# Performance work log

Measured on AMD Instinct MI355X. Metric: run time of the kernel, lower is better.

Reference implementation:

```python
import jax, jax.numpy as jnp
import numpy as np
from functools import partial

E = 256   # input_size (embedding dim)
H = 256   # hidden_size
T = 4096  # number of admissions (GRU sequence length, batch=1)


def _gru_seq(x_seq, w_ih, w_hh, b_ih, b_hh):
    """Single-layer unidirectional GRU over x_seq [T, E] with batch=1.
    PyTorch gate order: r, z, n. Returns outputs [T, H]."""
    h_dim = w_hh.shape[1]
    # input projections are step-independent: precompute [T, 3H]
    gi_all = x_seq @ w_ih.T + b_ih

    def step(h, gi):
        gh = h @ w_hh.T + b_hh
        i_r, i_z, i_n = jnp.split(gi, 3)
        h_r, h_z, h_n = jnp.split(gh, 3)
        r = jax.nn.sigmoid(i_r + h_r)
        z = jax.nn.sigmoid(i_z + h_z)
        n = jnp.tanh(i_n + r * h_n)
        h_new = (1.0 - z) * n + z * h
        return h_new, h_new

    h0 = jnp.zeros((h_dim,), x_seq.dtype)
    _, out = jax.lax.scan(step, h0, gi_all)
    return out  # [T, H]


def setup_inputs() -> dict:
    key = jax.random.key(0)
    ks = jax.random.split(key, 16)
    u = lambda k, shape, s: jax.random.uniform(k, shape, jnp.float32, -s, s)
    sg = 1.0 / np.sqrt(H)  # PyTorch GRU/Linear init scale
    inp = {}
    # embeddings initialized uniform(-0.1, 0.1) per initialize_weights()
    inp["emb_diag"] = u(ks[0], (20000, E), 0.1)
    inp["emb_proc"] = u(ks[1], (15000, E), 0.1)  # unused by forward (source bug), kept for fidelity
    # GRU params (layer 0), gate order r,z,n
    inp["wih_d"] = u(ks[2], (3 * H, E), sg)
    inp["whh_d"] = u(ks[3], (3 * H, H), sg)
    inp["bih_d"] = u(ks[4], (3 * H,), sg)
    inp["bhh_d"] = u(ks[5], (3 * H,), sg)
    inp["wih_p"] = u(ks[6], (3 * H, E), sg)
    inp["whh_p"] = u(ks[7], (3 * H, H), sg)
    inp["bih_p"] = u(ks[8], (3 * H,), sg)
    inp["bhh_p"] = u(ks[9], (3 * H,), sg)
    # linear_embedding: ReLU -> Linear(2H, H)
    sl = 1.0 / np.sqrt(2 * H)
    inp["w_lin"] = u(ks[10], (H, 2 * H), sl)
    inp["b_lin"] = u(ks[11], (H,), sl)
    # ragged admission code lists, represented as fixed-length rows
    inp["diag_codes"] = jax.random.randint(ks[12], (T, 32), 0, 20000)
    inp["proc_codes"] = jax.random.randint(ks[13], (T, 16), 0, 15000)
    inp["input_medication"] = jax.random.randint(ks[14], (T, 24), 0, 3000)
    return inp


def reference(emb_diag, emb_proc, wih_d, whh_d, bih_d, bhh_d,
              wih_p, whh_p, bih_p, bhh_p, w_lin, b_lin,
              diag_codes, proc_codes, input_medication):
    # per-admission embedding gather + mean pool (dropout rate 0 -> identity)
    # NOTE: original source uses embedding_diagnoses for BOTH loops (bug kept).
    seq_d = emb_diag[diag_codes].mean(axis=1)  # [T, E]
    seq_p = emb_diag[proc_codes].mean(axis=1)  # [T, E]
    out_d = _gru_seq(seq_d, wih_d, whh_d, bih_d, bhh_d)  # [T, H]
    out_p = _gru_seq(seq_p, wih_p, whh_p, bih_p, bhh_p)  # [T, H]
    patient = jnp.concatenate([out_d, out_p], axis=-1)   # [T, 2H]
    queries = jax.nn.relu(patient) @ w_lin.T + b_lin     # [T, H]
    query = queries[-1:]
    memory_keys = queries[:-1]
    memory_values = input_medication[:-1]
    return (query, memory_keys, memory_values)
```

## Files before the change

### kernel.cpp

```cpp
#include <hip/hip_runtime.h>
#include <hip/hip_fp16.h>

#define T_SEQ 4096
#define E_DIM 256
#define H_DIM 256
#define G3    768

#define KEYS_OFF 256
#define MED_OFF  1048576

#define WS_SEQ_D   0
#define WS_SEQ_P   1048576
#define WS_GI_D    2097152
#define WS_GI_P    5242880
#define WS_PATIENT 8388608

#define SW_SCALE   2016.0f
#define SH_SCALE   127.0f
#define INV_SY     (1.0f / (2016.0f * 127.0f))

__device__ __forceinline__ float fast_rcp(float x) {
#if __has_builtin(__builtin_amdgcn_rcpf)
    return __builtin_amdgcn_rcpf(x);
#else
    return 1.f / x;
#endif
}

__device__ __forceinline__ int sdot4(int a, int b, int c) {
#if __has_builtin(__builtin_amdgcn_sdot4)
    return __builtin_amdgcn_sdot4(a, b, c, false);
#else
    c += ((a << 24) >> 24) * ((b << 24) >> 24);
    c += ((a << 16) >> 24) * ((b << 16) >> 24);
    c += ((a <<  8) >> 24) * ((b <<  8) >> 24);
    c += ( a        >> 24) * ( b        >> 24);
    return c;
#endif
}

__device__ __forceinline__ int quad_sum_i32(int x) {
#if __has_builtin(__builtin_amdgcn_update_dpp)
    x += __builtin_amdgcn_update_dpp(0, x, 0xB1 , 0xF, 0xF, true);
    x += __builtin_amdgcn_update_dpp(0, x, 0x4E , 0xF, 0xF, true);
    return x;
#else
    x += __shfl_xor(x, 1);
    x += __shfl_xor(x, 2);
    return x;
#endif
}

__global__ __launch_bounds__(256) void gather_mean_kernel(
    const float* __restrict__ emb, const int* __restrict__ dcodes,
    const int* __restrict__ pcodes, const int* __restrict__ med,
    float* __restrict__ seq_d, float* __restrict__ seq_p,
    float* __restrict__ med_out)
{
    const int t = blockIdx.x;
    const int e = threadIdx.x;
    __shared__ int cd[32];
    __shared__ int cp[16];
    if (e < 32) cd[e] = dcodes[t * 32 + e];
    else if (e < 48) cp[e - 32] = pcodes[t * 16 + (e - 32)];
    __syncthreads();

    float sd = 0.f;
#pragma unroll 4
    for (int i = 0; i < 32; i++) sd += emb[(size_t)cd[i] * E_DIM + e];
    seq_d[(size_t)t * E_DIM + e] = sd * (1.f / 32.f);

    float sp = 0.f;
#pragma unroll 4
    for (int i = 0; i < 16; i++) sp += emb[(size_t)cp[i] * E_DIM + e];
    seq_p[(size_t)t * E_DIM + e] = sp * (1.f / 16.f);

    if (t < T_SEQ - 1 && e < 24) med_out[t * 24 + e] = (float)med[t * 24 + e];
}

__global__ __launch_bounds__(256) void gemm_gi_kernel(
    const float* __restrict__ seq_d, const float* __restrict__ seq_p,
    const float* __restrict__ wih_d, const float* __restrict__ wih_p,
    const float* __restrict__ bih_d, const float* __restrict__ bih_p,
    float* __restrict__ gi_d, float* __restrict__ gi_p)
{
    const int K = E_DIM, N = G3;
    const float* A    = blockIdx.z ? seq_p : seq_d;
    const float* W    = blockIdx.z ? wih_p : wih_d;
    const float* bias = blockIdx.z ? bih_p : bih_d;
    float*       C    = blockIdx.z ? gi_p  : gi_d;

    __shared__ float As[16][132];
    __shared__ float Bs[16][132];

    const int tid = threadIdx.x;
    const int tx = tid & 15, ty = tid >> 4;
    const int m0 = blockIdx.x * 128, n0 = blockIdx.y * 128;
    const int r = tid >> 2;
    const int c = (tid & 3) << 2;

    float acc[8][8];
#pragma unroll
    for (int i = 0; i < 8; i++)
#pragma unroll
        for (int j = 0; j < 8; j++) acc[i][j] = 0.f;

    for (int k0 = 0; k0 < K; k0 += 16) {
        float4 a0 = *(const float4*)&A[(size_t)(m0 + r) * K + k0 + c];
        float4 a1 = *(const float4*)&A[(size_t)(m0 + r + 64) * K + k0 + c];
        float4 b0 = *(const float4*)&W[(size_t)(n0 + r) * K + k0 + c];
        float4 b1 = *(const float4*)&W[(size_t)(n0 + r + 64) * K + k0 + c];
        As[c + 0][r] = a0.x; As[c + 1][r] = a0.y; As[c + 2][r] = a0.z; As[c + 3][r] = a0.w;
        As[c + 0][r + 64] = a1.x; As[c + 1][r + 64] = a1.y; As[c + 2][r + 64] = a1.z; As[c + 3][r + 64] = a1.w;
        Bs[c + 0][r] = b0.x; Bs[c + 1][r] = b0.y; Bs[c + 2][r] = b0.z; Bs[c + 3][r] = b0.w;
        Bs[c + 0][r + 64] = b1.x; Bs[c + 1][r + 64] = b1.y; Bs[c + 2][r + 64] = b1.z; Bs[c + 3][r + 64] = b1.w;
        __syncthreads();
#pragma unroll
        for (int k = 0; k < 16; k++) {
            float4 aa0 = *(const float4*)&As[k][ty * 8];
            float4 aa1 = *(const float4*)&As[k][ty * 8 + 4];
            float4 bb0 = *(const float4*)&Bs[k][tx * 8];
            float4 bb1 = *(const float4*)&Bs[k][tx * 8 + 4];
            float a[8] = {aa0.x, aa0.y, aa0.z, aa0.w, aa1.x, aa1.y, aa1.z, aa1.w};
            float b[8] = {bb0.x, bb0.y, bb0.z, bb0.w, bb1.x, bb1.y, bb1.z, bb1.w};
#pragma unroll
            for (int i = 0; i < 8; i++)
#pragma unroll
                for (int j = 0; j < 8; j++) acc[i][j] = fmaf(a[i], b[j], acc[i][j]);
        }
        __syncthreads();
    }

#pragma unroll
    for (int i = 0; i < 8; i++) {
        const int m = m0 + ty * 8 + i;
#pragma unroll
        for (int j = 0; j < 8; j++) {
            const int n = n0 + tx * 8 + j;
            C[(size_t)m * N + n] = acc[i][j] + bias[n];
        }
    }
}

__global__ __launch_bounds__(256) void quant_whh_kernel(
    const float* __restrict__ whh_d, const float* __restrict__ whh_p,
    unsigned int* __restrict__ w8_d, unsigned int* __restrict__ w8_p)
{
    const int idx = blockIdx.x * 256 + threadIdx.x;
    const float* src = blockIdx.y ? whh_p : whh_d;
    unsigned int* dst = blockIdx.y ? w8_p : w8_d;
    const float4 f = *(const float4*)&src[(size_t)idx * 4];
    const int b0 = (int)rintf(f.x * SW_SCALE) & 0xFF;
    const int b1 = (int)rintf(f.y * SW_SCALE) & 0xFF;
    const int b2 = (int)rintf(f.z * SW_SCALE) & 0xFF;
    const int b3 = (int)rintf(f.w * SW_SCALE) & 0xFF;
    dst[idx] = (unsigned int)(b0 | (b1 << 8) | (b2 << 16) | (b3 << 24));
}

__global__ __launch_bounds__(1024, 4) void gru_scan_kernel(
    const unsigned int* __restrict__ w8_d, const unsigned int* __restrict__ w8_p,
    const float* __restrict__ bhh_d, const float* __restrict__ bhh_p,
    const float* __restrict__ gi_d, const float* __restrict__ gi_p,
    float* __restrict__ patient)
{
    const unsigned int* w8 = blockIdx.x ? w8_p : w8_d;
    const float* bhh = blockIdx.x ? bhh_p : bhh_d;
    const float* gi  = blockIdx.x ? gi_p  : gi_d;
    const int col_off = blockIdx.x ? H_DIM : 0;

    const int tid = threadIdx.x;
    const int q = tid >> 2;
    const int l = tid & 3;

    int wreg[3][16];
#pragma unroll
    for (int g = 0; g < 3; g++) {
        const int4* p = (const int4*)(w8 + ((size_t)(g * 256 + q) * 64 + l * 16));
#pragma unroll
        for (int i = 0; i < 4; i++) {
            const int4 v = p[i];
            wreg[g][4 * i + 0] = v.x;
            wreg[g][4 * i + 1] = v.y;
            wreg[g][4 * i + 2] = v.z;
            wreg[g][4 * i + 3] = v.w;
        }
    }

    __shared__ __align__(16) char hb[4 * 80];
    __shared__ int ylds[3 * 256];

    if (tid < 320) hb[tid] = 0;

    float h = 0.f, g0 = 0.f, g1 = 0.f, g2 = 0.f, b0 = 0.f, b1 = 0.f, b2 = 0.f;
    if (tid < H_DIM) {
        b0 = bhh[tid]; b1 = bhh[256 + tid]; b2 = bhh[512 + tid];
        g0 = gi[tid]; g1 = gi[256 + tid]; g2 = gi[512 + tid];
    }
    __syncthreads();

    const uint4* hp = (const uint4*)(hb + l * 80);

    for (int t = 0; t < T_SEQ; t++) {
        const uint4 H0 = hp[0], H1 = hp[1], H2 = hp[2], H3 = hp[3];
        int a0 = 0, a1 = 0, a2 = 0;
        {
            const int hd0 = (int)H0.x, hd1 = (int)H0.y, hd2 = (int)H0.z, hd3 = (int)H0.w;
            const int hd4 = (int)H1.x, hd5 = (int)H1.y, hd6 = (int)H1.z, hd7 = (int)H1.w;
            const int hd8 = (int)H2.x, hd9 = (int)H2.y, hd10 = (int)H2.z, hd11 = (int)H2.w;
            const int hd12 = (int)H3.x, hd13 = (int)H3.y, hd14 = (int)H3.z, hd15 = (int)H3.w;
#define DOT_G(A, G) \
            A = sdot4(wreg[G][0],  hd0,  A); A = sdot4(wreg[G][1],  hd1,  A); \
            A = sdot4(wreg[G][2],  hd2,  A); A = sdot4(wreg[G][3],  hd3,  A); \
            A = sdot4(wreg[G][4],  hd4,  A); A = sdot4(wreg[G][5],  hd5,  A); \
            A = sdot4(wreg[G][6],  hd6,  A); A = sdot4(wreg[G][7],  hd7,  A); \
            A = sdot4(wreg[G][8],  hd8,  A); A = sdot4(wreg[G][9],  hd9,  A); \
            A = sdot4(wreg[G][10], hd10, A); A = sdot4(wreg[G][11], hd11, A); \
            A = sdot4(wreg[G][12], hd12, A); A = sdot4(wreg[G][13], hd13, A); \
            A = sdot4(wreg[G][14], hd14, A); A = sdot4(wreg[G][15], hd15, A);
            DOT_G(a0, 0)
            DOT_G(a1, 1)
            DOT_G(a2, 2)
#undef DOT_G
        }
        a0 = quad_sum_i32(a0);
        a1 = quad_sum_i32(a1);
        a2 = quad_sum_i32(a2);
        if (l == 0) {
            ylds[q] = a0;
            ylds[256 + q] = a1;
            ylds[512 + q] = a2;
        }
        __syncthreads();

        if (tid < H_DIM) {
            const float y0 = (float)ylds[tid] * INV_SY;
            const float y1 = (float)ylds[256 + tid] * INV_SY;
            const float y2 = (float)ylds[512 + tid] * INV_SY;
            const float xr = g0 + y0 + b0;
            const float xz = g1 + y1 + b1;
            const float r = fast_rcp(1.f + __expf(-xr));
            const float z = fast_rcp(1.f + __expf(-xz));
            float xn = g2 + r * (y2 + b2);
            xn = fminf(fmaxf(xn, -15.f), 15.f);
            const float e2 = __expf(2.f * xn);
            const float n = (e2 - 1.f) * fast_rcp(e2 + 1.f);
            h = (1.f - z) * n + z * h;
            hb[(tid >> 6) * 80 + (tid & 63)] = (char)(int)rintf(h * SH_SCALE);
            patient[(size_t)t * 512 + col_off + tid] = h;
            const int tn = (t < T_SEQ - 1) ? (t + 1) : t;
            g0 = gi[(size_t)tn * G3 + tid];
            g1 = gi[(size_t)tn * G3 + 256 + tid];
            g2 = gi[(size_t)tn * G3 + 512 + tid];
        }
        __syncthreads();
    }
}

__global__ __launch_bounds__(256) void gemm_fin_kernel(
    const float* __restrict__ patient, const float* __restrict__ w_lin,
    const float* __restrict__ b_lin, float* __restrict__ out)
{
    const int K = 512, N = H_DIM;

    __shared__ float As[16][132];
    __shared__ float Bs[16][132];

    const int tid = threadIdx.x;
    const int tx = tid & 15, ty = tid >> 4;
    const int m0 = blockIdx.x * 128, n0 = blockIdx.y * 128;
    const int r = tid >> 2;
    const int c = (tid & 3) << 2;

    float acc[8][8];
#pragma unroll
    for (int i = 0; i < 8; i++)
#pragma unroll
        for (int j = 0; j < 8; j++) acc[i][j] = 0.f;

    for (int k0 = 0; k0 < K; k0 += 16) {
        float4 a0 = *(const float4*)&patient[(size_t)(m0 + r) * K + k0 + c];
        float4 a1 = *(const float4*)&patient[(size_t)(m0 + r + 64) * K + k0 + c];
        float4 b0 = *(const float4*)&w_lin[(size_t)(n0 + r) * K + k0 + c];
        float4 b1 = *(const float4*)&w_lin[(size_t)(n0 + r + 64) * K + k0 + c];
        a0.x = fmaxf(a0.x, 0.f); a0.y = fmaxf(a0.y, 0.f); a0.z = fmaxf(a0.z, 0.f); a0.w = fmaxf(a0.w, 0.f);
        a1.x = fmaxf(a1.x, 0.f); a1.y = fmaxf(a1.y, 0.f); a1.z = fmaxf(a1.z, 0.f); a1.w = fmaxf(a1.w, 0.f);
        As[c + 0][r] = a0.x; As[c + 1][r] = a0.y; As[c + 2][r] = a0.z; As[c + 3][r] = a0.w;
        As[c + 0][r + 64] = a1.x; As[c + 1][r + 64] = a1.y; As[c + 2][r + 64] = a1.z; As[c + 3][r + 64] = a1.w;
        Bs[c + 0][r] = b0.x; Bs[c + 1][r] = b0.y; Bs[c + 2][r] = b0.z; Bs[c + 3][r] = b0.w;
        Bs[c + 0][r + 64] = b1.x; Bs[c + 1][r + 64] = b1.y; Bs[c + 2][r + 64] = b1.z; Bs[c + 3][r + 64] = b1.w;
        __syncthreads();
#pragma unroll
        for (int k = 0; k < 16; k++) {
            float4 aa0 = *(const float4*)&As[k][ty * 8];
            float4 aa1 = *(const float4*)&As[k][ty * 8 + 4];
            float4 bb0 = *(const float4*)&Bs[k][tx * 8];
            float4 bb1 = *(const float4*)&Bs[k][tx * 8 + 4];
            float a[8] = {aa0.x, aa0.y, aa0.z, aa0.w, aa1.x, aa1.y, aa1.z, aa1.w};
            float b[8] = {bb0.x, bb0.y, bb0.z, bb0.w, bb1.x, bb1.y, bb1.z, bb1.w};
#pragma unroll
            for (int i = 0; i < 8; i++)
#pragma unroll
                for (int j = 0; j < 8; j++) acc[i][j] = fmaf(a[i], b[j], acc[i][j]);
        }
        __syncthreads();
    }

#pragma unroll
    for (int i = 0; i < 8; i++) {
        const int m = m0 + ty * 8 + i;
#pragma unroll
        for (int j = 0; j < 8; j++) {
            const int n = n0 + tx * 8 + j;
            const float v = acc[i][j] + b_lin[n];
            if (m == T_SEQ - 1) out[n] = v;
            else out[KEYS_OFF + (size_t)m * H_DIM + n] = v;
        }
    }
}

extern "C" void kernel_launch(void* const* d_in, const int* in_sizes, int n_in,
                              void* d_out, int out_size, void* d_ws, size_t ws_size,
                              hipStream_t stream)
{
    const float* emb_diag = (const float*)d_in[0];
    const float* wih_d = (const float*)d_in[2];
    const float* whh_d = (const float*)d_in[3];
    const float* bih_d = (const float*)d_in[4];
    const float* bhh_d = (const float*)d_in[5];
    const float* wih_p = (const float*)d_in[6];
    const float* whh_p = (const float*)d_in[7];
    const float* bih_p = (const float*)d_in[8];
    const float* bhh_p = (const float*)d_in[9];
    const float* w_lin = (const float*)d_in[10];
    const float* b_lin = (const float*)d_in[11];
    const int* dcodes = (const int*)d_in[12];
    const int* pcodes = (const int*)d_in[13];
    const int* med    = (const int*)d_in[14];

    float* out = (float*)d_out;
    float* ws  = (float*)d_ws;

    float* seq_d   = ws + WS_SEQ_D;
    float* seq_p   = ws + WS_SEQ_P;
    float* gi_d    = ws + WS_GI_D;
    float* gi_p    = ws + WS_GI_P;
    float* patient = ws + WS_PATIENT;
    unsigned int* w8_d = (unsigned int*)(ws + WS_SEQ_D);
    unsigned int* w8_p = (unsigned int*)(ws + WS_SEQ_P);

    gather_mean_kernel<<<T_SEQ, 256, 0, stream>>>(
        emb_diag, dcodes, pcodes, med, seq_d, seq_p, out + MED_OFF);

    gemm_gi_kernel<<<dim3(32, 6, 2), 256, 0, stream>>>(
        seq_d, seq_p, wih_d, wih_p, bih_d, bih_p, gi_d, gi_p);

    quant_whh_kernel<<<dim3(192, 2), 256, 0, stream>>>(
        whh_d, whh_p, w8_d, w8_p);

    gru_scan_kernel<<<2, 1024, 0, stream>>>(
        w8_d, w8_p, bhh_d, bhh_p, gi_d, gi_p, patient);

    gemm_fin_kernel<<<dim3(32, 2, 1), 256, 0, stream>>>(
        patient, w_lin, b_lin, out);
}
```

Measured before the change: 2.993 ms.

## Double-buffer GRU hidden state to use one barrier per step

```diff
diff --git a/kernel.cpp b/kernel.cpp
--- a/kernel.cpp
+++ b/kernel.cpp
@@ -82,12 +82,14 @@
     const float* __restrict__ seq_d, const float* __restrict__ seq_p,
     const float* __restrict__ wih_d, const float* __restrict__ wih_p,
     const float* __restrict__ bih_d, const float* __restrict__ bih_p,
+    const float* __restrict__ bhh_d, const float* __restrict__ bhh_p,
     float* __restrict__ gi_d, float* __restrict__ gi_p)
 {
     const int K = E_DIM, N = G3;
     const float* A    = blockIdx.z ? seq_p : seq_d;
     const float* W    = blockIdx.z ? wih_p : wih_d;
     const float* bias = blockIdx.z ? bih_p : bih_d;
+    const float* bhh  = blockIdx.z ? bhh_p : bhh_d;
     float*       C    = blockIdx.z ? gi_p  : gi_d;
 
     __shared__ float As[16][132];
@@ -137,7 +139,8 @@
 #pragma unroll
         for (int j = 0; j < 8; j++) {
             const int n = n0 + tx * 8 + j;
-            C[(size_t)m * N + n] = acc[i][j] + bias[n];
+            const float bb = bias[n] + ((n < 512) ? bhh[n] : 0.f);
+            C[(size_t)m * N + n] = acc[i][j] + bb;
         }
     }
 }
@@ -186,74 +189,79 @@
         }
     }
 
-    __shared__ __align__(16) char hb[4 * 80];
-    __shared__ int ylds[3 * 256];
-
+    __shared__ __align__(16) char hb[640];
     if (tid < 320) hb[tid] = 0;
 
-    float h = 0.f, g0 = 0.f, g1 = 0.f, g2 = 0.f, b0 = 0.f, b1 = 0.f, b2 = 0.f;
-    if (tid < H_DIM) {
-        b0 = bhh[tid]; b1 = bhh[256 + tid]; b2 = bhh[512 + tid];
-        g0 = gi[tid]; g1 = gi[256 + tid]; g2 = gi[512 + tid];
-    }
+    const bool gl = (l == 0);
+    const int wq = (q >> 6) * 80 + (q & 63);
+
+    float h = 0.f, g0 = 0.f, g1 = 0.f, g2 = 0.f, b2 = 0.f;
+    if (gl) {
+        b2 = bhh[512 + q];
+        g0 = gi[q]; g1 = gi[256 + q]; g2 = gi[512 + q];
+    }
+    const float* gi_t = gi + G3;
+    float*       pat  = patient + col_off;
+
+    const char* hrd = hb + l * 80;
+
     __syncthreads();
 
-    const uint4* hp = (const uint4*)(hb + l * 80);
-
-    for (int t = 0; t < T_SEQ; t++) {
-        const uint4 H0 = hp[0], H1 = hp[1], H2 = hp[2], H3 = hp[3];
-        int a0 = 0, a1 = 0, a2 = 0;
-        {
-            const int hd0 = (int)H0.x, hd1 = (int)H0.y, hd2 = (int)H0.z, hd3 = (int)H0.w;
-            const int hd4 = (int)H1.x, hd5 = (int)H1.y, hd6 = (int)H1.z, hd7 = (int)H1.w;
-            const int hd8 = (int)H2.x, hd9 = (int)H2.y, hd10 = (int)H2.z, hd11 = (int)H2.w;
-            const int hd12 = (int)H3.x, hd13 = (int)H3.y, hd14 = (int)H3.z, hd15 = (int)H3.w;
+#define GRU_STEP(PAR)                                                          \
+    {                                                                          \
+        float ng0 = 0.f, ng1 = 0.f, ng2 = 0.f;                                 \
+        if (gl) { ng0 = gi_t[q]; ng1 = gi_t[256 + q]; ng2 = gi_t[512 + q]; }   \
+        const uint4 H0 = *(const uint4*)(hrd + (PAR)*320 + 0);                 \
+        const uint4 H1 = *(const uint4*)(hrd + (PAR)*320 + 16);                \
+        const uint4 H2 = *(const uint4*)(hrd + (PAR)*320 + 32);                \
+        const uint4 H3 = *(const uint4*)(hrd + (PAR)*320 + 48);                \
+        int a0 = 0, a1 = 0, a2 = 0;                                            \
+        const int hd0 = (int)H0.x, hd1 = (int)H0.y, hd2 = (int)H0.z, hd3 = (int)H0.w;   \
+        const int hd4 = (int)H1.x, hd5 = (int)H1.y, hd6 = (int)H1.z, hd7 = (int)H1.w;   \
+        const int hd8 = (int)H2.x, hd9 = (int)H2.y, hd10 = (int)H2.z, hd11 = (int)H2.w; \
+        const int hd12 = (int)H3.x, hd13 = (int)H3.y, hd14 = (int)H3.z, hd15 = (int)H3.w; \
+        DOT_G(a0, 0) DOT_G(a1, 1) DOT_G(a2, 2)                                 \
+        a0 = quad_sum_i32(a0);                                                 \
+        a1 = quad_sum_i32(a1);                                                 \
+        a2 = quad_sum_i32(a2);                                                 \
+        if (gl) {                                                              \
+            const float y0 = (float)a0 * INV_SY;                               \
+            const float y1 = (float)a1 * INV_SY;                               \
+            const float y2 = (float)a2 * INV_SY;                               \
+            const float xr = g0 + y0;                \
+            const float xz = g1 + y1;                \
+            const float r = fast_rcp(1.f + __expf(-xr));                       \
+            const float z = fast_rcp(1.f + __expf(-xz));                       \
+            float xn = g2 + r * (y2 + b2);                                     \
+            xn = fminf(fmaxf(xn, -15.f), 15.f);                                \
+            const float e2 = __expf(2.f * xn);                                 \
+            const float n = (e2 - 1.f) * fast_rcp(e2 + 1.f);                   \
+            h = (1.f - z) * n + z * h;                                         \
+            hb[((PAR) ^ 1) * 320 + wq] = (char)(int)rintf(h * SH_SCALE);       \
+            pat[q] = h;                                                        \
+            g0 = ng0; g1 = ng1; g2 = ng2;                                      \
+        }                                                                      \
+        gi_t += G3;                                                            \
+        pat += 512;                                                            \
+        __syncthreads();                                                       \
+    }
+
 #define DOT_G(A, G) \
-            A = sdot4(wreg[G][0],  hd0,  A); A = sdot4(wreg[G][1],  hd1,  A); \
-            A = sdot4(wreg[G][2],  hd2,  A); A = sdot4(wreg[G][3],  hd3,  A); \
-            A = sdot4(wreg[G][4],  hd4,  A); A = sdot4(wreg[G][5],  hd5,  A); \
-            A = sdot4(wreg[G][6],  hd6,  A); A = sdot4(wreg[G][7],  hd7,  A); \
-            A = sdot4(wreg[G][8],  hd8,  A); A = sdot4(wreg[G][9],  hd9,  A); \
-            A = sdot4(wreg[G][10], hd10, A); A = sdot4(wreg[G][11], hd11, A); \
-            A = sdot4(wreg[G][12], hd12, A); A = sdot4(wreg[G][13], hd13, A); \
-            A = sdot4(wreg[G][14], hd14, A); A = sdot4(wreg[G][15], hd15, A);
-            DOT_G(a0, 0)
-            DOT_G(a1, 1)
-            DOT_G(a2, 2)
+    A = sdot4(wreg[G][0],  hd0,  A); A = sdot4(wreg[G][1],  hd1,  A); \
+    A = sdot4(wreg[G][2],  hd2,  A); A = sdot4(wreg[G][3],  hd3,  A); \
+    A = sdot4(wreg[G][4],  hd4,  A); A = sdot4(wreg[G][5],  hd5,  A); \
+    A = sdot4(wreg[G][6],  hd6,  A); A = sdot4(wreg[G][7],  hd7,  A); \
+    A = sdot4(wreg[G][8],  hd8,  A); A = sdot4(wreg[G][9],  hd9,  A); \
+    A = sdot4(wreg[G][10], hd10, A); A = sdot4(wreg[G][11], hd11, A); \
+    A = sdot4(wreg[G][12], hd12, A); A = sdot4(wreg[G][13], hd13, A); \
+    A = sdot4(wreg[G][14], hd14, A); A = sdot4(wreg[G][15], hd15, A);
+
+    for (int t = 0; t < T_SEQ; t += 2) {
+        GRU_STEP(0)
+        GRU_STEP(1)
+    }
 #undef DOT_G
-        }
-        a0 = quad_sum_i32(a0);
-        a1 = quad_sum_i32(a1);
-        a2 = quad_sum_i32(a2);
-        if (l == 0) {
-            ylds[q] = a0;
-            ylds[256 + q] = a1;
-            ylds[512 + q] = a2;
-        }
-        __syncthreads();
-
-        if (tid < H_DIM) {
-            const float y0 = (float)ylds[tid] * INV_SY;
-            const float y1 = (float)ylds[256 + tid] * INV_SY;
-            const float y2 = (float)ylds[512 + tid] * INV_SY;
-            const float xr = g0 + y0 + b0;
-            const float xz = g1 + y1 + b1;
-            const float r = fast_rcp(1.f + __expf(-xr));
-            const float z = fast_rcp(1.f + __expf(-xz));
-            float xn = g2 + r * (y2 + b2);
-            xn = fminf(fmaxf(xn, -15.f), 15.f);
-            const float e2 = __expf(2.f * xn);
-            const float n = (e2 - 1.f) * fast_rcp(e2 + 1.f);
-            h = (1.f - z) * n + z * h;
-            hb[(tid >> 6) * 80 + (tid & 63)] = (char)(int)rintf(h * SH_SCALE);
-            patient[(size_t)t * 512 + col_off + tid] = h;
-            const int tn = (t < T_SEQ - 1) ? (t + 1) : t;
-            g0 = gi[(size_t)tn * G3 + tid];
-            g1 = gi[(size_t)tn * G3 + 256 + tid];
-            g2 = gi[(size_t)tn * G3 + 512 + tid];
-        }
-        __syncthreads();
-    }
+#undef GRU_STEP
 }
 
 __global__ __launch_bounds__(256) void gemm_fin_kernel(
@@ -352,7 +360,7 @@
         emb_diag, dcodes, pcodes, med, seq_d, seq_p, out + MED_OFF);
 
     gemm_gi_kernel<<<dim3(32, 6, 2), 256, 0, stream>>>(
-        seq_d, seq_p, wih_d, wih_p, bih_d, bih_p, gi_d, gi_p);
+        seq_d, seq_p, wih_d, wih_p, bih_d, bih_p, bhh_d, bhh_p, gi_d, gi_p);
 
     quant_whh_kernel<<<dim3(192, 2), 256, 0, stream>>>(
         whh_d, whh_p, w8_d, w8_p);
```

Measured after the change: 3.853 ms. 28.7% more time.
